# Kernel optimization log

Hardware: AMD Instinct MI355X
Metric: run time of the kernel (lower is better)

Reference implementation:

```python
import jax, jax.numpy as jnp
import numpy as np

H, S, D = 64, 64, 4096  # num_heads, head_size, hidden_size (D = H*S)
EPS = 1e-5


def setup_inputs() -> dict:
    key = jax.random.key(0)
    ks = jax.random.split(key, 20)
    n = lambda i, shape, s=1.0: s * jax.random.normal(ks[i], shape, dtype=jnp.float32)
    u = lambda i, shape: jax.random.uniform(ks[i], shape, dtype=jnp.float32)
    return {
        "x": n(0, (D,)),
        "state1": n(1, (D,)),
        "state2": n(2, (H, S, S), 0.1),
        "time_mix_k": u(3, (D,)),
        "time_mix_v": u(4, (D,)),
        "time_mix_r": u(5, (D,)),
        "time_mix_g": u(6, (D,)),
        # time_decay = exp(-exp(raw)) in (0,1); time_first = exp(raw) (time_faaaa-style, kept small)
        "time_decay": jnp.exp(-jnp.exp(n(7, (H, S, 1), 0.5))),
        "time_first": 0.3 * u(8, (H, S, 1)),
        "Wr": n(9, (D, D), 0.02),
        "Wk": n(10, (D, D), 0.01),   # key.weight / 2 baked in
        "Wv": n(11, (D, D), 0.005),  # value.weight / 4 baked in
        "Wg": n(12, (D, D), 0.02),
        "Wo": n(13, (D, D), 0.02),
        "ln1_w": 1.0 + n(14, (D,), 0.1),
        "ln1_b": n(15, (D,), 0.1),
        "lnx_w": 1.0 + n(16, (D,), 0.1),
        "lnx_b": n(17, (D,), 0.1),
    }


def reference(x, state1, state2, time_mix_k, time_mix_v, time_mix_r, time_mix_g,
              time_decay, time_first, Wr, Wk, Wv, Wg, Wo,
              ln1_w, ln1_b, lnx_w, lnx_b):
    last_x = x
    # ln_1 (nn.LayerNorm affine is identity-init; explicit w/b applied after)
    m = jnp.mean(x)
    var = jnp.mean((x - m) ** 2)
    xx = (x - m) * jax.lax.rsqrt(var + EPS) * ln1_w + ln1_b
    state1_out = xx

    mix = lambda t: state1 * (1.0 - t) + xx * t
    r = (Wr @ mix(time_mix_r)).reshape(H, 1, S)
    k = (Wk @ mix(time_mix_k)).reshape(H, S, 1)
    v = (Wv @ mix(time_mix_v)).reshape(H, 1, S)
    g_lin = Wg @ mix(time_mix_g)
    gate = g_lin * jax.nn.sigmoid(g_lin)  # SiLU

    kv = jnp.matmul(k, v)                              # [H, S, S] outer products
    wkv = jnp.matmul(r, kv * time_first + state2)       # [H, 1, S]
    state2_out = kv + state2 * time_decay

    # InstanceNorm2d over (1, S) spatial dims per head, no affine, biased var
    mu = jnp.mean(wkv, axis=(1, 2), keepdims=True)
    vv = jnp.mean((wkv - mu) ** 2, axis=(1, 2), keepdims=True)
    xn = ((wkv - mu) * jax.lax.rsqrt(vv + EPS)).reshape(D)
    y = (xn * lnx_w + lnx_b) * gate
    out = last_x + Wo @ y
    return (out, state1_out, state2_out)
```

## Files before the change

kernel.cpp:

```cpp
#include <hip/hip_runtime.h>
#include <math.h>

#define D 4096
#define H 64
#define S 64
#define EPS 1e-5f

__device__ __forceinline__ float wave_reduce_sum(float v) {
#pragma unroll
    for (int off = 32; off > 0; off >>= 1) v += __shfl_down(v, off, 64);
    return v;
}

__global__ __launch_bounds__(1024) void k_ln_mix(
    const float* __restrict__ x, const float* __restrict__ state1,
    const float* __restrict__ tmk, const float* __restrict__ tmv,
    const float* __restrict__ tmr, const float* __restrict__ tmg,
    const float* __restrict__ ln1w, const float* __restrict__ ln1b,
    float* __restrict__ state1_out, float* __restrict__ mix ) {
    __shared__ float red[32];
    __shared__ float mb[2];
    const int tid = threadIdx.x;
    const float4 xv = ((const float4*)x)[tid];
    float s = (xv.x + xv.y) + (xv.z + xv.w);
    float sq = (xv.x * xv.x + xv.y * xv.y) + (xv.z * xv.z + xv.w * xv.w);
    s = wave_reduce_sum(s);
    sq = wave_reduce_sum(sq);
    const int wave = tid >> 6, lane = tid & 63;
    if (lane == 0) { red[wave] = s; red[16 + wave] = sq; }
    __syncthreads();
    if (tid == 0) {
        float ts = 0.f, tq = 0.f;
        for (int i = 0; i < 16; ++i) { ts += red[i]; tq += red[16 + i]; }
        float m = ts / (float)D;
        float var = tq / (float)D - m * m;
        mb[0] = m;
        mb[1] = rsqrtf(var + EPS);
    }
    __syncthreads();
    const float m = mb[0], rs = mb[1];
    const float4 w4 = ((const float4*)ln1w)[tid];
    const float4 b4 = ((const float4*)ln1b)[tid];
    float4 xx;
    xx.x = (xv.x - m) * rs * w4.x + b4.x;
    xx.y = (xv.y - m) * rs * w4.y + b4.y;
    xx.z = (xv.z - m) * rs * w4.z + b4.z;
    xx.w = (xv.w - m) * rs * w4.w + b4.w;
    ((float4*)state1_out)[tid] = xx;
    const float4 s1 = ((const float4*)state1)[tid];
    float4 d;
    d.x = xx.x - s1.x; d.y = xx.y - s1.y; d.z = xx.z - s1.z; d.w = xx.w - s1.w;
    const float4 tr = ((const float4*)tmr)[tid];
    const float4 tk = ((const float4*)tmk)[tid];
    const float4 tv = ((const float4*)tmv)[tid];
    const float4 tg = ((const float4*)tmg)[tid];
    float4 o;
    o.x = s1.x + d.x * tr.x; o.y = s1.y + d.y * tr.y; o.z = s1.z + d.z * tr.z; o.w = s1.w + d.w * tr.w;
    ((float4*)mix)[tid] = o;
    o.x = s1.x + d.x * tk.x; o.y = s1.y + d.y * tk.y; o.z = s1.z + d.z * tk.z; o.w = s1.w + d.w * tk.w;
    ((float4*)mix)[1024 + tid] = o;
    o.x = s1.x + d.x * tv.x; o.y = s1.y + d.y * tv.y; o.z = s1.z + d.z * tv.z; o.w = s1.w + d.w * tv.w;
    ((float4*)mix)[2048 + tid] = o;
    o.x = s1.x + d.x * tg.x; o.y = s1.y + d.y * tg.y; o.z = s1.z + d.z * tg.z; o.w = s1.w + d.w * tg.w;
    ((float4*)mix)[3072 + tid] = o;
}

__global__ __launch_bounds__(256) void k_gemv4(
    const float* __restrict__ Wr, const float* __restrict__ Wk,
    const float* __restrict__ Wv, const float* __restrict__ Wg,
    const float* __restrict__ mix, float* __restrict__ rkvg) {
    __shared__ float4 smix[1024];
    const int wave = threadIdx.x >> 6, lane = threadIdx.x & 63;
    const int wg = blockIdx.x * 4 + wave;
    const int m = wg >> 11;
    const int r0 = (wg & 2047) * 2;
    const float* W = (m == 0) ? Wr : (m == 1) ? Wk : (m == 2) ? Wv : Wg;
    const float4* vx = (const float4*)mix + (m << 10);
#pragma unroll
    for (int t = 0; t < 4; ++t) smix[t * 256 + threadIdx.x] = vx[t * 256 + threadIdx.x];
    __syncthreads();
    const float4* w0p = (const float4*)W + (size_t)r0 * 1024;
    const float4* w1p = w0p + 1024;
    const int s = wg & 15;
    float4 pa[2], pb[2];
    pa[0] = w0p[s * 64 + lane];
    pb[0] = w1p[s * 64 + lane];
    pa[1] = w0p[((s + 1) & 15) * 64 + lane];
    pb[1] = w1p[((s + 1) & 15) * 64 + lane];
    float a0 = 0.f, a1 = 0.f, b0 = 0.f, b1 = 0.f;
#pragma unroll
    for (int it = 0; it < 16; ++it) {
        float4 wa = pa[it & 1], wb = pb[it & 1];
        if (it < 14) {
            const int cl = (s + it + 2) & 15;
            pa[it & 1] = w0p[cl * 64 + lane];
            pb[it & 1] = w1p[cl * 64 + lane];
        }
        const float4 xv = smix[((s + it) & 15) * 64 + lane];
        a0 += wa.x * xv.x + wa.y * xv.y;
        a1 += wa.z * xv.z + wa.w * xv.w;
        b0 += wb.x * xv.x + wb.y * xv.y;
        b1 += wb.z * xv.z + wb.w * xv.w;
    }
    float a = wave_reduce_sum(a0 + a1);
    float b = wave_reduce_sum(b0 + b1);
    if (lane == 0) {
        rkvg[m * D + r0] = a;
        rkvg[m * D + r0 + 1] = b;
    }
}

__global__ __launch_bounds__(1024) void k_heads(
    const float* __restrict__ rkvg, const float* __restrict__ state2,
    const float* __restrict__ tdecay, const float* __restrict__ tfirst,
    const float* __restrict__ lnxw, const float* __restrict__ lnxb,
    float* __restrict__ state2_out, float* __restrict__ y) {
    __shared__ float part[16][64];
    const int h = blockIdx.x;
    const int wave = threadIdx.x >> 6, j = threadIdx.x & 63;
    const int base = h * S;
    const float rj = rkvg[base + j];
    const float kj = rkvg[D + base + j];
    const float vj = rkvg[2 * D + base + j];
    const float tfj = tfirst[base + j];
    const float tdj = tdecay[base + j];
    const float* s2 = state2 + (size_t)h * S * S;
    float* s2o = state2_out + (size_t)h * S * S;
    float sv[4];
#pragma unroll
    for (int ii = 0; ii < 4; ++ii) sv[ii] = s2[(wave * 4 + ii) * S + j];
    float wkv = 0.f;
#pragma unroll
    for (int ii = 0; ii < 4; ++ii) {
        const int i = wave * 4 + ii;
        float ri = __shfl(rj, i, 64);
        float ki = __shfl(kj, i, 64);
        float tfi = __shfl(tfj, i, 64);
        float tdi = __shfl(tdj, i, 64);
        float kv = ki * vj;
        wkv += ri * (kv * tfi + sv[ii]);
        s2o[i * S + j] = kv + sv[ii] * tdi;
    }
    part[wave][j] = wkv;
    __syncthreads();
    if (wave == 0) {
        float w0 = 0.f;
#pragma unroll
        for (int t = 0; t < 16; ++t) w0 += part[t][j];
        float sum = w0, sq = w0 * w0;
#pragma unroll
        for (int off = 1; off < 64; off <<= 1) {
            sum += __shfl_xor(sum, off, 64);
            sq += __shfl_xor(sq, off, 64);
        }
        float mu = sum / (float)S;
        float var = sq / (float)S - mu * mu;
        float xn = (w0 - mu) * rsqrtf(var + EPS);
        float gj = rkvg[3 * D + base + j];
        float gate = gj / (1.f + expf(-gj));
        y[base + j] = (xn * lnxw[base + j] + lnxb[base + j]) * gate;
    }
}

__global__ __launch_bounds__(256) void k_out(
    const float* __restrict__ Wo, const float* __restrict__ y,
    const float* __restrict__ x, float* __restrict__ out) {
    __shared__ float4 sy[1024];
    const int wave = threadIdx.x >> 6, lane = threadIdx.x & 63;
    const int wg = blockIdx.x * 4 + wave;
    const float4* vy = (const float4*)y;
#pragma unroll
    for (int t = 0; t < 4; ++t) sy[t * 256 + threadIdx.x] = vy[t * 256 + threadIdx.x];
    __syncthreads();
    const float4* wp = (const float4*)Wo + (size_t)wg * 1024;
    const int s = wg & 15;
    float4 p[4];
#pragma unroll
    for (int u = 0; u < 4; ++u) p[u] = wp[((s + u) & 15) * 64 + lane];
    float a0 = 0.f, a1 = 0.f;
#pragma unroll
    for (int it = 0; it < 16; ++it) {
        const float4 w = p[it & 3];
        if (it < 12) {
            const int cl = (s + it + 4) & 15;
            p[it & 3] = wp[cl * 64 + lane];
        }
        const float4 xv = sy[((s + it) & 15) * 64 + lane];
        a0 += w.x * xv.x + w.y * xv.y;
        a1 += w.z * xv.z + w.w * xv.w;
    }
    float a = wave_reduce_sum(a0 + a1);
    if (lane == 0) out[wg] = x[wg] + a;
}

extern "C" void kernel_launch(void* const* d_in, const int* in_sizes, int n_in,
                              void* d_out, int out_size, void* d_ws, size_t ws_size,
                              hipStream_t stream) {
    const float* x      = (const float*)d_in[0];
    const float* state1 = (const float*)d_in[1];
    const float* state2 = (const float*)d_in[2];
    const float* tmk    = (const float*)d_in[3];
    const float* tmv    = (const float*)d_in[4];
    const float* tmr    = (const float*)d_in[5];
    const float* tmg    = (const float*)d_in[6];
    const float* tdecay = (const float*)d_in[7];
    const float* tfirst = (const float*)d_in[8];
    const float* Wr     = (const float*)d_in[9];
    const float* Wk     = (const float*)d_in[10];
    const float* Wv     = (const float*)d_in[11];
    const float* Wg     = (const float*)d_in[12];
    const float* Wo     = (const float*)d_in[13];
    const float* ln1w   = (const float*)d_in[14];
    const float* ln1b   = (const float*)d_in[15];
    const float* lnxw   = (const float*)d_in[16];
    const float* lnxb   = (const float*)d_in[17];

    float* out        = (float*)d_out;
    float* state1_out = out + D;
    float* state2_out = out + 2 * D;

    float* mix  = (float*)d_ws;
    float* rkvg = mix + 4 * D;
    float* y    = rkvg + 4 * D;

    k_ln_mix<<<1, 1024, 0, stream>>>(x, state1, tmk, tmv, tmr, tmg, ln1w, ln1b,
                                     state1_out, mix);
    k_gemv4<<<2048, 256, 0, stream>>>(Wr, Wk, Wv, Wg, mix, rkvg);
    k_heads<<<64, 1024, 0, stream>>>(rkvg, state2, tdecay, tfirst, lnxw, lnxb,
                                     state2_out, y);
    k_out<<<1024, 256, 0, stream>>>(Wo, y, x, out);
}
```

Before: 325.9 us.

## Issue all weight-row loads upfront before barrier in GEMV kernels, one row per wave

Both GEMV kernels now have each wave load its entire 16-float4 weight row into registers in one burst, fenced by scheduling barriers. These loads are issued before the __syncthreads that waits for the shared-memory vector staging, so the weight fetch overlaps the staging. The fused r/k/v/g GEMV changes from two rows per wave to one, which doubles its grid. The goal is more memory-level parallelism on a bandwidth-bound GEMV. The cost is higher register pressure and dropping the staggered column start, which may cause more DRAM channel contention.

```diff
diff --git a/kernel.cpp b/kernel.cpp
--- a/kernel.cpp
+++ b/kernel.cpp
@@ -72,42 +72,28 @@
     __shared__ float4 smix[1024];
     const int wave = threadIdx.x >> 6, lane = threadIdx.x & 63;
     const int wg = blockIdx.x * 4 + wave;
-    const int m = wg >> 11;
-    const int r0 = (wg & 2047) * 2;
+    const int m = wg >> 12;
+    const int row = wg & 4095;
     const float* W = (m == 0) ? Wr : (m == 1) ? Wk : (m == 2) ? Wv : Wg;
     const float4* vx = (const float4*)mix + (m << 10);
 #pragma unroll
     for (int t = 0; t < 4; ++t) smix[t * 256 + threadIdx.x] = vx[t * 256 + threadIdx.x];
-    __syncthreads();
-    const float4* w0p = (const float4*)W + (size_t)r0 * 1024;
-    const float4* w1p = w0p + 1024;
-    const int s = wg & 15;
-    float4 pa[2], pb[2];
-    pa[0] = w0p[s * 64 + lane];
-    pb[0] = w1p[s * 64 + lane];
-    pa[1] = w0p[((s + 1) & 15) * 64 + lane];
-    pb[1] = w1p[((s + 1) & 15) * 64 + lane];
-    float a0 = 0.f, a1 = 0.f, b0 = 0.f, b1 = 0.f;
-#pragma unroll
-    for (int it = 0; it < 16; ++it) {
-        float4 wa = pa[it & 1], wb = pb[it & 1];
-        if (it < 14) {
-            const int cl = (s + it + 2) & 15;
-            pa[it & 1] = w0p[cl * 64 + lane];
-            pb[it & 1] = w1p[cl * 64 + lane];
-        }
-        const float4 xv = smix[((s + it) & 15) * 64 + lane];
-        a0 += wa.x * xv.x + wa.y * xv.y;
-        a1 += wa.z * xv.z + wa.w * xv.w;
-        b0 += wb.x * xv.x + wb.y * xv.y;
-        b1 += wb.z * xv.z + wb.w * xv.w;
+    const float4* wp = (const float4*)W + (size_t)row * 1024;
+    float4 wv[16];
+    __builtin_amdgcn_sched_barrier(0);
+#pragma unroll
+    for (int u = 0; u < 16; ++u) wv[u] = wp[u * 64 + lane];
+    __builtin_amdgcn_sched_barrier(0);
+    __syncthreads();
+    float a0 = 0.f, a1 = 0.f;
+#pragma unroll
+    for (int u = 0; u < 16; ++u) {
+        const float4 xv = smix[u * 64 + lane];
+        a0 += wv[u].x * xv.x + wv[u].y * xv.y;
+        a1 += wv[u].z * xv.z + wv[u].w * xv.w;
     }
     float a = wave_reduce_sum(a0 + a1);
-    float b = wave_reduce_sum(b0 + b1);
-    if (lane == 0) {
-        rkvg[m * D + r0] = a;
-        rkvg[m * D + r0 + 1] = b;
-    }
+    if (lane == 0) rkvg[m * D + row] = a;
 }
 
 __global__ __launch_bounds__(1024) void k_heads(
@@ -167,30 +153,26 @@
     const float* __restrict__ x, float* __restrict__ out) {
     __shared__ float4 sy[1024];
     const int wave = threadIdx.x >> 6, lane = threadIdx.x & 63;
-    const int wg = blockIdx.x * 4 + wave;
+    const int row = blockIdx.x * 4 + wave;
     const float4* vy = (const float4*)y;
 #pragma unroll
     for (int t = 0; t < 4; ++t) sy[t * 256 + threadIdx.x] = vy[t * 256 + threadIdx.x];
-    __syncthreads();
-    const float4* wp = (const float4*)Wo + (size_t)wg * 1024;
-    const int s = wg & 15;
-    float4 p[4];
-#pragma unroll
-    for (int u = 0; u < 4; ++u) p[u] = wp[((s + u) & 15) * 64 + lane];
+    const float4* wp = (const float4*)Wo + (size_t)row * 1024;
+    float4 wv[16];
+    __builtin_amdgcn_sched_barrier(0);
+#pragma unroll
+    for (int u = 0; u < 16; ++u) wv[u] = wp[u * 64 + lane];
+    __builtin_amdgcn_sched_barrier(0);
+    __syncthreads();
     float a0 = 0.f, a1 = 0.f;
 #pragma unroll
-    for (int it = 0; it < 16; ++it) {
-        const float4 w = p[it & 3];
-        if (it < 12) {
-            const int cl = (s + it + 4) & 15;
-            p[it & 3] = wp[cl * 64 + lane];
-        }
-        const float4 xv = sy[((s + it) & 15) * 64 + lane];
-        a0 += w.x * xv.x + w.y * xv.y;
-        a1 += w.z * xv.z + w.w * xv.w;
+    for (int u = 0; u < 16; ++u) {
+        const float4 xv = sy[u * 64 + lane];
+        a0 += wv[u].x * xv.x + wv[u].y * xv.y;
+        a1 += wv[u].z * xv.z + wv[u].w * xv.w;
     }
     float a = wave_reduce_sum(a0 + a1);
-    if (lane == 0) out[wg] = x[wg] + a;
+    if (lane == 0) out[row] = x[row] + a;
 }
 
 extern "C" void kernel_launch(void* const* d_in, const int* in_sizes, int n_in,
@@ -225,7 +207,7 @@
 
     k_ln_mix<<<1, 1024, 0, stream>>>(x, state1, tmk, tmv, tmr, tmg, ln1w, ln1b,
                                      state1_out, mix);
-    k_gemv4<<<2048, 256, 0, stream>>>(Wr, Wk, Wv, Wg, mix, rkvg);
+    k_gemv4<<<4096, 256, 0, stream>>>(Wr, Wk, Wv, Wg, mix, rkvg);
     k_heads<<<64, 1024, 0, stream>>>(rkvg, state2, tdecay, tfirst, lnxw, lnxb,
                                      state2_out, y);
     k_out<<<1024, 256, 0, stream>>>(Wo, y, x, out);
```

Result: no change. 326.8 us (+0.3%).
